# Performance work log

Measured on AMD Instinct MI355X. Metric: run time of the kernel, lower is better.

The kernel has to match this reference:

```python
import jax, jax.numpy as jnp
import numpy as np

NEG_SLOPE = 0.2  # PyG GATConv default leaky_relu slope
N_NODES, N_EDGES, F_IN, HID = 25000, 200000, 64, 128


def gat_layer(x, src, dst, W, a_src, a_dst, b, heads, ch):
    """PyG-style GATConv (concat=True, eval mode). x:[N,Fin] -> [N,heads*ch]."""
    N = x.shape[0]
    h = (x @ W).reshape(N, heads, ch)                      # [N,H,C]
    al_s = jnp.sum(h * a_src, axis=-1)                     # [N,H]
    al_d = jnp.sum(h * a_dst, axis=-1)                     # [N,H]
    e = jax.nn.leaky_relu(al_s[src] + al_d[dst], NEG_SLOPE)  # [E,H]
    # segment softmax over incoming edges of each dst node (stable)
    e = e - jax.ops.segment_max(e, dst, num_segments=N)[dst]
    ex = jnp.exp(e)
    alpha = ex / jax.ops.segment_sum(ex, dst, num_segments=N)[dst]  # [E,H]
    out = jax.ops.segment_sum(h[src] * alpha[:, :, None], dst, num_segments=N)  # [N,H,C]
    return out.reshape(N, heads * ch) + b


def setup_inputs() -> dict:
    key = jax.random.key(0)
    ks = jax.random.split(key, 24)
    def g(k, shape, fan_in):
        return jax.random.normal(k, shape, dtype=jnp.float32) / np.sqrt(fan_in)
    inp = {
        "x": jax.random.normal(ks[0], (N_NODES, F_IN), dtype=jnp.float32),
        "edge_index": jax.random.randint(ks[1], (2, N_EDGES), 0, N_NODES, dtype=jnp.int64) if jax.config.jax_enable_x64 else jax.random.randint(ks[1], (2, N_EDGES), 0, N_NODES).astype(jnp.int32),
        "liquor_idx": jax.random.randint(ks[2], (4096,), 0, N_NODES),
        "ingredient_idx": jax.random.randint(ks[3], (4096,), 0, N_NODES),
        "W1": g(ks[4], (F_IN, 8 * HID), F_IN), "a_s1": g(ks[5], (8, HID), HID), "a_d1": g(ks[6], (8, HID), HID), "b1": jnp.zeros((8 * HID,), jnp.float32),
        "W2": g(ks[7], (8 * HID, 8 * HID), 8 * HID), "a_s2": g(ks[8], (8, HID), HID), "a_d2": g(ks[9], (8, HID), HID), "b2": jnp.zeros((8 * HID,), jnp.float32),
        "W3": g(ks[10], (8 * HID, HID), 8 * HID), "a_s3": g(ks[11], (1, HID), HID), "a_d3": g(ks[12], (1, HID), HID), "b3": jnp.zeros((HID,), jnp.float32),
        # MLP scorer: 256 -> 128 -> 64 -> 1
        "mw1": g(ks[13], (2 * HID, HID), 2 * HID), "mb1": jnp.zeros((HID,), jnp.float32),
        "mw2": g(ks[14], (HID, HID // 2), HID), "mb2": jnp.zeros((HID // 2,), jnp.float32),
        "mw3": g(ks[15], (HID // 2, 1), HID // 2), "mb3": jnp.zeros((1,), jnp.float32),
    }
    return inp


def reference(x, edge_index, liquor_idx, ingredient_idx,
              W1, a_s1, a_d1, b1, W2, a_s2, a_d2, b2, W3, a_s3, a_d3, b3,
              mw1, mb1, mw2, mb2, mw3, mb3):
    N = x.shape[0]
    loops = jnp.arange(N, dtype=edge_index.dtype)  # GATConv adds self-loops
    src = jnp.concatenate([edge_index[0], loops])
    dst = jnp.concatenate([edge_index[1], loops])
    h = jax.nn.relu(gat_layer(x, src, dst, W1, a_s1, a_d1, b1, 8, HID))
    h = jax.nn.relu(gat_layer(h, src, dst, W2, a_s2, a_d2, b2, 8, HID))
    h = gat_layer(h, src, dst, W3, a_s3, a_d3, b3, 1, HID)
    pair = jnp.concatenate([h[liquor_idx], h[ingredient_idx]], axis=-1)  # [B,256]
    z = jax.nn.relu(pair @ mw1 + mb1)
    z = jax.nn.relu(z @ mw2 + mb2)
    z = z @ mw3 + mb3
    return jax.nn.sigmoid(z).squeeze(-1)
```

## Files before the change

kernel.cpp:

```cpp
#include <hip/hip_runtime.h>
#include <math.h>

#define NEG_SLOPE 0.2f

typedef short short8 __attribute__((ext_vector_type(8)));
typedef float f32x4 __attribute__((ext_vector_type(4)));

__device__ __forceinline__ float lrelu(float x){ return x > 0.f ? x : NEG_SLOPE * x; }

__device__ __forceinline__ unsigned short f2bf(float f){
  union { float f; unsigned u; } v; v.f = f;
  unsigned r = v.u + 0x7fff + ((v.u >> 16) & 1);
  return (unsigned short)(r >> 16);
}
__device__ __forceinline__ float bf2f(unsigned short u){
  union { unsigned u; float f; } v; v.u = ((unsigned)u) << 16; return v.f;
}

__device__ __forceinline__ void gld16(const unsigned short* g, unsigned short* l){
  __builtin_amdgcn_global_load_lds(
      (const __attribute__((address_space(1))) unsigned int*)g,
      (__attribute__((address_space(3))) unsigned int*)l, 16, 0, 0);
}

#define MFMA_BF16 __builtin_amdgcn_mfma_f32_16x16x32_bf16

__global__ void k_count(const int* __restrict__ dst, int* __restrict__ cnt, int E){
  int e = blockIdx.x*blockDim.x + threadIdx.x;
  if (e < E) atomicAdd(&cnt[dst[e]], 1);
}

__global__ void k_blockscan(const int* __restrict__ cnt, int* __restrict__ row,
                            int* __restrict__ aux, int n){
  __shared__ int buf[256];
  int t = threadIdx.x;
  int base = blockIdx.x * 256;
  int v = (base + t < n) ? cnt[base + t] : 0;
  buf[t] = v;
  __syncthreads();
  #pragma unroll
  for (int off = 1; off < 256; off <<= 1){
    int u = (t >= off) ? buf[t - off] : 0;
    __syncthreads();
    buf[t] += u;
    __syncthreads();
  }
  if (base + t < n) row[base + t + 1] = buf[t];
  if (t == 255) aux[blockIdx.x] = buf[255];
  if (blockIdx.x == 0 && t == 0) row[0] = 0;
}

__global__ void k_addoff(const int* __restrict__ aux, int* __restrict__ row, int n){
  __shared__ int s_pre;
  int b = blockIdx.x, t = threadIdx.x;
  if (t == 0){
    int pre = 0;
    for (int i = 0; i < b; ++i) pre += aux[i];
    s_pre = pre;
  }
  __syncthreads();
  int i = b * 256 + t;
  if (i < n) row[i + 1] += s_pre;
}

__global__ void k_scatter(const int* __restrict__ src, const int* __restrict__ dst,
                          const int* __restrict__ row, int* __restrict__ cur,
                          int* __restrict__ csr, int E){
  int e = blockIdx.x*blockDim.x + threadIdx.x;
  if (e < E){
    int d = dst[e];
    int p = atomicAdd(&cur[d], 1);
    csr[row[d] + p] = src[e];
  }
}

__global__ void k_prep(const float* __restrict__ x, unsigned short* __restrict__ xb, int nx, int nxb,
                       const float* __restrict__ W1, unsigned short* __restrict__ Wt1,
                       const float* __restrict__ W2, unsigned short* __restrict__ Wt2,
                       const float* __restrict__ W3, unsigned short* __restrict__ Wt3){
  __shared__ float tile[32][33];
  int b = blockIdx.x, t = threadIdx.x;
  if (b < nxb){
    int i0 = b * 2048 + t * 8;
    if (i0 + 8 <= nx){
      float4 f0 = *reinterpret_cast<const float4*>(x + i0);
      float4 f1 = *reinterpret_cast<const float4*>(x + i0 + 4);
      short8 o;
      o[0]=f2bf(f0.x); o[1]=f2bf(f0.y); o[2]=f2bf(f0.z); o[3]=f2bf(f0.w);
      o[4]=f2bf(f1.x); o[5]=f2bf(f1.y); o[6]=f2bf(f1.z); o[7]=f2bf(f1.w);
      *reinterpret_cast<short8*>(xb + i0) = o;
    } else {
      for (int k = 0; k < 8 && i0 + k < nx; ++k) xb[i0 + k] = f2bf(x[i0 + k]);
    }
    return;
  }
  const float* W; unsigned short* Wt; int K, N, ti;
  if (b < nxb + 64)            { W = W1; Wt = Wt1; K = 64;   N = 1024; ti = b - nxb;
                                 int kb = (ti & 1) * 32, nb = (ti >> 1) * 32;
                                 int tx = t & 31, ty = t >> 5;
                                 #pragma unroll
                                 for (int i = ty; i < 32; i += 8) tile[i][tx] = W[(size_t)(kb+i)*N + nb+tx];
                                 __syncthreads();
                                 #pragma unroll
                                 for (int i = ty; i < 32; i += 8) Wt[(size_t)(nb+i)*K + kb+tx] = f2bf(tile[tx][i]);
                                 return; }
  if (b < nxb + 64 + 1024)     { W = W2; Wt = Wt2; K = 1024; N = 1024; ti = b - nxb - 64; }
  else                         { W = W3; Wt = Wt3; K = 1024; N = 128;  ti = b - nxb - 64 - 1024; }
  int kb = (ti & 31) * 32, nb = (ti >> 5) * 32;
  int tx = t & 31, ty = t >> 5;
  #pragma unroll
  for (int i = ty; i < 32; i += 8) tile[i][tx] = W[(size_t)(kb+i)*N + nb+tx];
  __syncthreads();
  #pragma unroll
  for (int i = ty; i < 32; i += 8) Wt[(size_t)(nb+i)*K + kb+tx] = f2bf(tile[tx][i]);
}

__global__ void k_fold(const float* __restrict__ W1, const float* __restrict__ a_s,
                       const float* __restrict__ a_d, float* __restrict__ ws){
  int k = blockIdx.x, t = threadIdx.x;
  int h = t >> 5, l = t & 31;
  float4 wv = *reinterpret_cast<const float4*>(&W1[(size_t)k * 1024 + h * 128 + l * 4]);
  float4 sv = *reinterpret_cast<const float4*>(&a_s[h * 128 + l * 4]);
  float4 dv = *reinterpret_cast<const float4*>(&a_d[h * 128 + l * 4]);
  float ps = wv.x*sv.x + wv.y*sv.y + wv.z*sv.z + wv.w*sv.w;
  float pd = wv.x*dv.x + wv.y*dv.y + wv.z*dv.z + wv.w*dv.w;
  #pragma unroll
  for (int off = 16; off >= 1; off >>= 1){
    ps += __shfl_xor(ps, off);
    pd += __shfl_xor(pd, off);
  }
  if (l == 0){ ws[k * 16 + h] = ps; ws[k * 16 + 8 + h] = pd; }
}

__global__ void k_logits1(const unsigned short* __restrict__ xb, const float* __restrict__ ws,
                          float* __restrict__ ALS, float* __restrict__ ALD, int N){
  __shared__ unsigned short lx[32 * 64];
  __shared__ float lw[64 * 16];
  int t = threadIdx.x;
  int n0 = blockIdx.x * 32;
  int r = t >> 3, c = (t & 7) * 8;
  if (n0 + r < N)
    *reinterpret_cast<short8*>(&lx[r * 64 + c]) =
      *reinterpret_cast<const short8*>(&xb[(size_t)(n0 + r) * 64 + c]);
  else {
    short8 z = {0,0,0,0,0,0,0,0};
    *reinterpret_cast<short8*>(&lx[r * 64 + c]) = z;
  }
  *reinterpret_cast<float4*>(&lw[t * 4]) = *reinterpret_cast<const float4*>(&ws[t * 4]);
  __syncthreads();
  int nl = t >> 3, h = t & 7;
  if (n0 + nl >= N) return;
  float s = 0.f, d = 0.f;
  #pragma unroll 8
  for (int k = 0; k < 64; ++k){
    float xv = bf2f(lx[nl * 64 + k]);
    s = fmaf(xv, lw[k * 16 + h], s);
    d = fmaf(xv, lw[k * 16 + 8 + h], d);
  }
  ALS[(size_t)(n0 + nl) * 8 + h] = s;
  ALD[(size_t)(n0 + nl) * 8 + h] = d;
}

__global__ void k_gat_x(const unsigned short* __restrict__ xb, const float* __restrict__ ALS,
                        const float* __restrict__ ALD, const int* __restrict__ row,
                        const int* __restrict__ csr, unsigned short* __restrict__ G, int N){
  int t = threadIdx.x;
  int n = blockIdx.x * 4 + (t >> 6);
  if (n >= N) return;
  int lane = t & 63;
  float ald[8], m[8], l[8], acc[8];
  float xv = bf2f(xb[(size_t)n * 64 + lane]);
  #pragma unroll
  for (int h = 0; h < 8; ++h){
    ald[h] = ALD[(size_t)n * 8 + h];
    m[h] = lrelu(ALS[(size_t)n * 8 + h] + ald[h]);
    l[h] = 1.f;
    acc[h] = xv;
  }
  int beg = row[n], end = row[n + 1];
  for (int j = beg; j < end; ++j){
    int s = csr[j];
    float xs = bf2f(xb[(size_t)s * 64 + lane]);
    #pragma unroll
    for (int h = 0; h < 8; ++h){
      float e = lrelu(ALS[(size_t)s * 8 + h] + ald[h]);
      float mn = fmaxf(m[h], e);
      float sc = __expf(m[h] - mn);
      float p  = __expf(e - mn);
      acc[h] = acc[h] * sc + p * xs;
      l[h]   = l[h] * sc + p;
      m[h]   = mn;
    }
  }
  #pragma unroll
  for (int h = 0; h < 8; ++h)
    G[(size_t)n * 512 + h * 64 + lane] = f2bf(acc[h] / l[h]);
}

__global__ __launch_bounds__(256) void k_gemm_g(
    const unsigned short* __restrict__ G,
    const unsigned short* __restrict__ Bt,
    const float* __restrict__ bias,
    unsigned short* __restrict__ C,
    int M){
  __shared__ unsigned short As[128 * 32];
  __shared__ unsigned short Bs[128 * 32];
  const int nwg = gridDim.x;
  int bid = blockIdx.x;
  int swz = ((nwg & 7) == 0) ? ((bid & 7) * (nwg >> 3) + (bid >> 3)) : bid;
  const int head = swz % 8, byi = swz / 8;
  const int bm = byi * 128, bn = head * 128;
  const int tid  = threadIdx.x;
  const int lane = tid & 63, wave = tid >> 6;
  const int wr = wave >> 1, wc = wave & 1;
  const int lr = lane & 15, lk = lane >> 4;
  const int srow = wave * 16 + (lane >> 2);
  const int skc  = (lane & 3) * 8;
  int ar0 = bm + srow;      if (ar0 >= M) ar0 = M - 1;
  int ar1 = bm + srow + 64; if (ar1 >= M) ar1 = M - 1;
  const unsigned short* ga0 = G + (size_t)ar0 * 512 + head * 64 + skc;
  const unsigned short* ga1 = G + (size_t)ar1 * 512 + head * 64 + skc;
  const unsigned short* gb0 = Bt + (size_t)(bn + srow) * 64 + skc;
  const unsigned short* gb1 = Bt + (size_t)(bn + srow + 64) * 64 + skc;
  f32x4 acc[4][4] = {};
  #pragma unroll
  for (int k0 = 0; k0 < 64; k0 += 32){
    gld16(ga0 + k0, &As[(size_t)wave * 512]);
    gld16(ga1 + k0, &As[(size_t)(wave + 4) * 512]);
    gld16(gb0 + k0, &Bs[(size_t)wave * 512]);
    gld16(gb1 + k0, &Bs[(size_t)(wave + 4) * 512]);
    __syncthreads();
    short8 af[4], bg[4];
    #pragma unroll
    for (int m = 0; m < 4; ++m)
      af[m] = *reinterpret_cast<const short8*>(&As[(wr * 64 + m * 16 + lr) * 32 + lk * 8]);
    #pragma unroll
    for (int n = 0; n < 4; ++n)
      bg[n] = *reinterpret_cast<const short8*>(&Bs[(wc * 64 + n * 16 + lr) * 32 + lk * 8]);
    #pragma unroll
    for (int m = 0; m < 4; ++m)
      #pragma unroll
      for (int n = 0; n < 4; ++n)
        acc[m][n] = MFMA_BF16(af[m], bg[n], acc[m][n], 0, 0, 0);
    __syncthreads();
  }
  float bv[4];
  #pragma unroll
  for (int n = 0; n < 4; ++n) bv[n] = bias[bn + wc * 64 + n * 16 + lr];
  #pragma unroll
  for (int m = 0; m < 4; ++m){
    #pragma unroll
    for (int j = 0; j < 4; ++j){
      int rowi = bm + wr * 64 + m * 16 + lk * 4 + j;
      if (rowi < M){
        #pragma unroll
        for (int n = 0; n < 4; ++n)
          C[(size_t)rowi * 1024 + bn + wc * 64 + n * 16 + lr] = f2bf(fmaxf(acc[m][n][j] + bv[n], 0.f));
      }
    }
  }
}

template<int HEADS>
__global__ __launch_bounds__(256) void k_gemm_fused(
    const unsigned short* __restrict__ A, const unsigned short* __restrict__ Bt,
    unsigned short* __restrict__ C,
    const float* __restrict__ a_s, const float* __restrict__ a_d,
    float* __restrict__ ALS, float* __restrict__ ALD,
    int M, int N, int K, int gxc){
  __shared__ unsigned short SMEM[2 * 128 * 32];
  unsigned short* As = SMEM;
  unsigned short* Bs = SMEM + 128 * 32;
  const int nwg = gridDim.x;
  int bid = blockIdx.x;
  int swz = ((nwg & 7) == 0) ? ((bid & 7) * (nwg >> 3) + (bid >> 3)) : bid;
  const int bxi = swz % gxc, byi = swz / gxc;
  const int bm = byi * 128, bn = bxi * 128;
  const int head = bxi;
  const int tid  = threadIdx.x;
  const int lane = tid & 63, wave = tid >> 6;
  const int wr = wave >> 1, wc = wave & 1;
  const int lr = lane & 15, lk = lane >> 4;
  const int srow = wave * 16 + (lane >> 2);
  const int skc  = (lane & 3) * 8;
  int ar0 = bm + srow;      if (ar0 >= M) ar0 = M - 1;
  int ar1 = bm + srow + 64; if (ar1 >= M) ar1 = M - 1;
  const unsigned short* ga0 = A  + (size_t)ar0 * K + skc;
  const unsigned short* ga1 = A  + (size_t)ar1 * K + skc;
  const unsigned short* gb0 = Bt + (size_t)(bn + srow) * K + skc;
  const unsigned short* gb1 = Bt + (size_t)(bn + srow + 64) * K + skc;
  f32x4 acc[4][4] = {};
  for (int k0 = 0; k0 < K; k0 += 32){
    gld16(ga0 + k0, &As[(size_t)wave * 512]);
    gld16(ga1 + k0, &As[(size_t)(wave + 4) * 512]);
    gld16(gb0 + k0, &Bs[(size_t)wave * 512]);
    gld16(gb1 + k0, &Bs[(size_t)(wave + 4) * 512]);
    __syncthreads();
    short8 af[4], bg[4];
    #pragma unroll
    for (int m = 0; m < 4; ++m)
      af[m] = *reinterpret_cast<const short8*>(&As[(wr * 64 + m * 16 + lr) * 32 + lk * 8]);
    #pragma unroll
    for (int n = 0; n < 4; ++n)
      bg[n] = *reinterpret_cast<const short8*>(&Bs[(wc * 64 + n * 16 + lr) * 32 + lk * 8]);
    #pragma unroll
    for (int m = 0; m < 4; ++m)
      #pragma unroll
      for (int n = 0; n < 4; ++n)
        acc[m][n] = MFMA_BF16(af[m], bg[n], acc[m][n], 0, 0, 0);
    __syncthreads();
  }
  #pragma unroll
  for (int m = 0; m < 4; ++m){
    #pragma unroll
    for (int j = 0; j < 4; ++j){
      int rowi = bm + wr * 64 + m * 16 + lk * 4 + j;
      if (rowi < M){
        #pragma unroll
        for (int n = 0; n < 4; ++n)
          C[(size_t)rowi * N + bn + wc * 64 + n * 16 + lr] = f2bf(acc[m][n][j]);
      }
    }
  }
  float as4[4], ad4[4];
  #pragma unroll
  for (int n = 0; n < 4; ++n){
    as4[n] = a_s[head * 128 + wc * 64 + n * 16 + lr];
    ad4[n] = a_d[head * 128 + wc * 64 + n * 16 + lr];
  }
  float* red = (float*)SMEM;
  #pragma unroll
  for (int m = 0; m < 4; ++m){
    #pragma unroll
    for (int j = 0; j < 4; ++j){
      float ps = 0.f;
      #pragma unroll
      for (int n = 0; n < 4; ++n) ps = fmaf(acc[m][n][j], as4[n], ps);
      red[(wr * 64 + m * 16 + lk * 4 + j) * 32 + wc * 16 + lr] = ps;
    }
  }
  __syncthreads();
  if (tid < 128){
    float s = 0.f;
    #pragma unroll
    for (int i = 0; i < 32; ++i) s += red[tid * 32 + ((i + tid) & 31)];
    int gr = bm + tid;
    if (gr < M) ALS[(size_t)gr * HEADS + head] = s;
  }
  __syncthreads();
  #pragma unroll
  for (int m = 0; m < 4; ++m){
    #pragma unroll
    for (int j = 0; j < 4; ++j){
      float pd = 0.f;
      #pragma unroll
      for (int n = 0; n < 4; ++n) pd = fmaf(acc[m][n][j], ad4[n], pd);
      red[(wr * 64 + m * 16 + lk * 4 + j) * 32 + wc * 16 + lr] = pd;
    }
  }
  __syncthreads();
  if (tid < 128){
    float s = 0.f;
    #pragma unroll
    for (int i = 0; i < 32; ++i) s += red[tid * 32 + ((i + tid) & 31)];
    int gr = bm + tid;
    if (gr < M) ALD[(size_t)gr * HEADS + head] = s;
  }
}

__global__ __launch_bounds__(512, 2) void k_gemm256p8(
    const unsigned short* __restrict__ A,
    const unsigned short* __restrict__ Bt,
    unsigned short* __restrict__ C,
    const float* __restrict__ a_s, const float* __restrict__ a_d,
    float* __restrict__ ALS, float* __restrict__ ALD,
    int M, int N, int K, int gxc){
  __shared__ unsigned short smem[2 * 32768];
  const int nwg = gridDim.x;
  int bid = blockIdx.x;
  int swz = ((nwg & 7) == 0) ? ((bid & 7) * (nwg >> 3) + (bid >> 3)) : bid;
  const int bxi = swz % gxc, byi = swz / gxc;
  const int bm = byi * 256, bn = bxi * 256;
  const int tid = threadIdx.x;
  const int lane = tid & 63, wave = tid >> 6;
  const int wr = wave >> 2, wc = wave & 3;
  const int lr = lane & 15, lk = lane >> 4;
  const int sr = tid >> 3;
  const int scol = ((tid & 7) << 3) ^ ((sr & 7) << 3);
  unsigned offA[4], offB[4];
  #pragma unroll
  for (int u = 0; u < 4; ++u){
    int r = bm + u * 64 + sr; if (r >= M) r = M - 1;
    offA[u] = (unsigned)r * (unsigned)K + scol;
    offB[u] = (unsigned)(bn + u * 64 + sr) * (unsigned)K + scol;
  }
  const int wdst = wave * 512;
  const int NKT = K >> 6;
  const int NIT = NKT >> 1;

  #define STA(T,u) gld16(A  + (size_t)offA[u] + (size_t)(T)*64, &smem[((T)&1)*32768 + (u)*4096 + wdst])
  #define STB(T,u) gld16(Bt + (size_t)offB[u] + (size_t)(T)*64, &smem[((T)&1)*32768 + 16384 + (u)*4096 + wdst])

  #pragma unroll
  for (int u = 0; u < 4; ++u) STA(0, u);
  #pragma unroll
  for (int u = 0; u < 4; ++u) STB(0, u);
  #pragma unroll
  for (int u = 0; u < 4; ++u) STA(1, u);
  asm volatile("s_waitcnt vmcnt(4)" ::: "memory");
  __builtin_amdgcn_s_barrier();

  f32x4 acc[8][4] = {};
  short8 af[4][2], bg[4][2];

  #define RD_A(moff) \
    _Pragma("unroll") \
    for (int m = 0; m < 4; ++m){ \
      int row = wr * 128 + (m + (moff)) * 16 + lr; \
      int rb = row * 64, sw = (row & 7) << 3; \
      af[m][0] = *reinterpret_cast<const short8*>(&sa[rb + ((lk * 8) ^ sw)]); \
      af[m][1] = *reinterpret_cast<const short8*>(&sa[rb + ((32 + lk * 8) ^ sw)]); \
    }
  #define RD_B(n0_, n1_) \
    _Pragma("unroll") \
    for (int n = (n0_); n < (n1_); ++n){ \
      int row = wc * 64 + n * 16 + lr; \
      int rb = row * 64, sw = (row & 7) << 3; \
      bg[n][0] = *reinterpret_cast<const short8*>(&sb[rb + ((lk * 8) ^ sw)]); \
      bg[n][1] = *reinterpret_cast<const short8*>(&sb[rb + ((32 + lk * 8) ^ sw)]); \
    }
  #define SYNC_MFMA_BEG \
    __builtin_amdgcn_s_barrier(); \
    asm volatile("s_waitcnt lgkmcnt(0)" ::: "memory"); \
    __builtin_amdgcn_sched_barrier(0); \
    __builtin_amdgcn_s_setprio(1);
  #define QUAD(mb, nb) \
    _Pragma("unroll") \
    for (int m = 0; m < 4; ++m) \
      _Pragma("unroll") \
      for (int n = 0; n < 2; ++n){ \
        acc[(mb)+m][(nb)+n] = MFMA_BF16(af[m][0], bg[(nb)+n][0], acc[(mb)+m][(nb)+n], 0, 0, 0); \
        acc[(mb)+m][(nb)+n] = MFMA_BF16(af[m][1], bg[(nb)+n][1], acc[(mb)+m][(nb)+n], 0, 0, 0); \
      }
  #define SYNC_MFMA_END \
    __builtin_amdgcn_s_setprio(0); \
    __builtin_amdgcn_s_barrier();

  for (int it = 0; it < NIT; ++it){
    const int T = it << 1;
    {
      const unsigned short* sa = &smem[(T & 1) * 32768];
      const unsigned short* sb = sa + 16384;
      RD_A(0); RD_B(0, 2);
      STB(T + 1, 0); STB(T + 1, 1);
      SYNC_MFMA_BEG; QUAD(0, 0); SYNC_MFMA_END;
      RD_B(2, 4);
      STB(T + 1, 2); STB(T + 1, 3);
      SYNC_MFMA_BEG; QUAD(0, 2); SYNC_MFMA_END;
      RD_A(4);
      if (T + 2 < NKT){ STA(T + 2, 0); STA(T + 2, 2); }
      SYNC_MFMA_BEG; QUAD(4, 0); SYNC_MFMA_END;
      if (T + 2 < NKT){ STA(T + 2, 1); STA(T + 2, 3); }
      __builtin_amdgcn_s_barrier();
      __builtin_amdgcn_s_setprio(1);
      QUAD(4, 2);
      __builtin_amdgcn_s_setprio(0);
      asm volatile("s_waitcnt vmcnt(4)" ::: "memory");
      __builtin_amdgcn_s_barrier();
    }
    {
      const unsigned short* sa = &smem[((T + 1) & 1) * 32768];
      const unsigned short* sb = sa + 16384;
      RD_A(0); RD_B(0, 2);
      if (T + 2 < NKT){ STB(T + 2, 0); STB(T + 2, 1); }
      SYNC_MFMA_BEG; QUAD(0, 0); SYNC_MFMA_END;
      RD_B(2, 4);
      if (T + 2 < NKT){ STB(T + 2, 2); STB(T + 2, 3); }
      SYNC_MFMA_BEG; QUAD(0, 2); SYNC_MFMA_END;
      RD_A(4);
      if (T + 3 < NKT){ STA(T + 3, 0); STA(T + 3, 2); }
      SYNC_MFMA_BEG; QUAD(4, 0); SYNC_MFMA_END;
      if (T + 3 < NKT){ STA(T + 3, 1); STA(T + 3, 3); }
      __builtin_amdgcn_s_barrier();
      __builtin_amdgcn_s_setprio(1);
      QUAD(4, 2);
      __builtin_amdgcn_s_setprio(0);
      asm volatile("s_waitcnt vmcnt(4)" ::: "memory");
      __builtin_amdgcn_s_barrier();
    }
  }

  #pragma unroll
  for (int m = 0; m < 8; ++m){
    #pragma unroll
    for (int j = 0; j < 4; ++j){
      int row = bm + wr * 128 + m * 16 + lk * 4 + j;
      if (row < M){
        #pragma unroll
        for (int n = 0; n < 4; ++n)
          C[(size_t)row * N + bn + wc * 64 + n * 16 + lr] = f2bf(acc[m][n][j]);
      }
    }
  }
  const int hloc = wc >> 1;
  float as4[4], ad4[4];
  #pragma unroll
  for (int n = 0; n < 4; ++n){
    as4[n] = a_s[(bxi * 2 + hloc) * 128 + (wc & 1) * 64 + n * 16 + lr];
    ad4[n] = a_d[(bxi * 2 + hloc) * 128 + (wc & 1) * 64 + n * 16 + lr];
  }
  float2* red = (float2*)smem;
  __syncthreads();
  #pragma unroll
  for (int hh = 0; hh < 2; ++hh){
    if (hloc == hh){
      #pragma unroll
      for (int m = 0; m < 8; ++m){
        #pragma unroll
        for (int j = 0; j < 4; ++j){
          float ps = 0.f, pd = 0.f;
          #pragma unroll
          for (int n = 0; n < 4; ++n){
            ps = fmaf(acc[m][n][j], as4[n], ps);
            pd = fmaf(acc[m][n][j], ad4[n], pd);
          }
          red[(wr * 128 + m * 16 + lk * 4 + j) * 32 + (wc & 1) * 16 + lr] = make_float2(ps, pd);
        }
      }
    }
    __syncthreads();
    if (tid < 256){
      float ss = 0.f, sd = 0.f;
      #pragma unroll
      for (int i = 0; i < 32; ++i){
        float2 v = red[tid * 32 + ((i + tid) & 31)];
        ss += v.x; sd += v.y;
      }
      int gr = bm + tid;
      if (gr < M){
        ALS[(size_t)gr * 8 + bxi * 2 + hh] = ss;
        ALD[(size_t)gr * 8 + bxi * 2 + hh] = sd;
      }
    }
    __syncthreads();
  }
  #undef STA
  #undef STB
  #undef RD_A
  #undef RD_B
  #undef SYNC_MFMA_BEG
  #undef QUAD
  #undef SYNC_MFMA_END
}

template<int HEADS, int VEC, int OUTBF>
__global__ void k_gat_bf(const unsigned short* __restrict__ hp, const float* __restrict__ al_s,
                         const float* __restrict__ al_d, const int* __restrict__ row,
                         const int* __restrict__ csr, const float* __restrict__ bias,
                         void* __restrict__ outv, int N, int do_relu){
  constexpr int TPH = 128 / VEC;
  int n = blockIdx.x;
  int t = threadIdx.x;
  int h = t / TPH;
  int c0 = (t % TPH) * VEC;
  float ald = al_d[(size_t)n * HEADS + h];
  float mA = lrelu(al_s[(size_t)n * HEADS + h] + ald);
  float lA = 1.f;
  float accA[VEC], accB[VEC];
  float mB = -1e30f, lB = 0.f;
  const unsigned short* hpn = hp + ((size_t)n * HEADS + h) * 128 + c0;
  if constexpr (VEC == 8){
    short8 hv8 = *reinterpret_cast<const short8*>(hpn);
    #pragma unroll
    for (int v = 0; v < 8; ++v){ accA[v] = bf2f((unsigned short)hv8[v]); accB[v] = 0.f; }
  } else {
    ushort2 hv2 = *reinterpret_cast<const ushort2*>(hpn);
    accA[0] = bf2f(hv2.x); accA[1] = bf2f(hv2.y);
    accB[0] = 0.f; accB[1] = 0.f;
  }
  int beg = row[n], end = row[n + 1];
  int j = beg;
  for (; j + 1 < end; j += 2){
    int s0 = csr[j], s1 = csr[j + 1];
    float e0 = lrelu(al_s[(size_t)s0 * HEADS + h] + ald);
    float e1 = lrelu(al_s[(size_t)s1 * HEADS + h] + ald);
    const unsigned short* p0 = hp + ((size_t)s0 * HEADS + h) * 128 + c0;
    const unsigned short* p1 = hp + ((size_t)s1 * HEADS + h) * 128 + c0;
    if constexpr (VEC == 8){
      short8 v0 = *reinterpret_cast<const short8*>(p0);
      short8 v1 = *reinterpret_cast<const short8*>(p1);
      float mn0 = fmaxf(mA, e0), mn1 = fmaxf(mB, e1);
      float sc0 = __expf(mA - mn0), sc1 = __expf(mB - mn1);
      float pw0 = __expf(e0 - mn0), pw1 = __expf(e1 - mn1);
      #pragma unroll
      for (int v = 0; v < 8; ++v){
        accA[v] = accA[v] * sc0 + pw0 * bf2f((unsigned short)v0[v]);
        accB[v] = accB[v] * sc1 + pw1 * bf2f((unsigned short)v1[v]);
      }
      lA = lA * sc0 + pw0; mA = mn0;
      lB = lB * sc1 + pw1; mB = mn1;
    } else {
      ushort2 v0 = *reinterpret_cast<const ushort2*>(p0);
      ushort2 v1 = *reinterpret_cast<const ushort2*>(p1);
      float mn0 = fmaxf(mA, e0), mn1 = fmaxf(mB, e1);
      float sc0 = __expf(mA - mn0), sc1 = __expf(mB - mn1);
      float pw0 = __expf(e0 - mn0), pw1 = __expf(e1 - mn1);
      accA[0] = accA[0] * sc0 + pw0 * bf2f(v0.x);
      accA[1] = accA[1] * sc0 + pw0 * bf2f(v0.y);
      accB[0] = accB[0] * sc1 + pw1 * bf2f(v1.x);
      accB[1] = accB[1] * sc1 + pw1 * bf2f(v1.y);
      lA = lA * sc0 + pw0; mA = mn0;
      lB = lB * sc1 + pw1; mB = mn1;
    }
  }
  if (j < end){
    int s0 = csr[j];
    float e0 = lrelu(al_s[(size_t)s0 * HEADS + h] + ald);
    const unsigned short* p0 = hp + ((size_t)s0 * HEADS + h) * 128 + c0;
    float mn0 = fmaxf(mA, e0);
    float sc0 = __expf(mA - mn0), pw0 = __expf(e0 - mn0);
    if constexpr (VEC == 8){
      short8 v0 = *reinterpret_cast<const short8*>(p0);
      #pragma unroll
      for (int v = 0; v < 8; ++v) accA[v] = accA[v] * sc0 + pw0 * bf2f((unsigned short)v0[v]);
    } else {
      ushort2 v0 = *reinterpret_cast<const ushort2*>(p0);
      accA[0] = accA[0] * sc0 + pw0 * bf2f(v0.x);
      accA[1] = accA[1] * sc0 + pw0 * bf2f(v0.y);
    }
    lA = lA * sc0 + pw0; mA = mn0;
  }
  float mn = fmaxf(mA, mB);
  float sA = __expf(mA - mn), sB = __expf(mB - mn);
  float l = lA * sA + lB * sB;
  float inv = 1.f / l;
  size_t ob = ((size_t)n * HEADS + h) * 128 + c0;
  #pragma unroll
  for (int v = 0; v < VEC; ++v){
    float o = (accA[v] * sA + accB[v] * sB) * inv + bias[h * 128 + c0 + v];
    if (do_relu) o = fmaxf(o, 0.f);
    if constexpr (OUTBF) ((unsigned short*)outv)[ob + v] = f2bf(o);
    else                 ((float*)outv)[ob + v] = o;
  }
}

__global__ void k_gat3(const unsigned short* __restrict__ hp, const float* __restrict__ al_s,
                       const float* __restrict__ al_d, const int* __restrict__ row,
                       const int* __restrict__ csr, const float* __restrict__ bias,
                       const int* __restrict__ liq, const int* __restrict__ ing,
                       float* __restrict__ out, int NB){
  int b = blockIdx.x;
  int n = (b < NB) ? liq[b] : ing[b - NB];
  int t = threadIdx.x;
  int c0 = t * 2;
  float ald = al_d[n];
  float m = lrelu(al_s[n] + ald);
  float l = 1.f;
  ushort2 hv2 = *reinterpret_cast<const ushort2*>(hp + (size_t)n * 128 + c0);
  float a0 = bf2f(hv2.x), a1 = bf2f(hv2.y);
  int beg = row[n], end = row[n + 1];
  for (int j = beg; j < end; ++j){
    int s = csr[j];
    float e = lrelu(al_s[s] + ald);
    float mn = fmaxf(m, e);
    float sc = __expf(m - mn), p = __expf(e - mn);
    ushort2 v = *reinterpret_cast<const ushort2*>(hp + (size_t)s * 128 + c0);
    a0 = a0 * sc + p * bf2f(v.x);
    a1 = a1 * sc + p * bf2f(v.y);
    l = l * sc + p;
    m = mn;
  }
  float inv = 1.f / l;
  out[(size_t)b * 128 + c0]     = a0 * inv + bias[c0];
  out[(size_t)b * 128 + c0 + 1] = a1 * inv + bias[c0 + 1];
}

__global__ void k_mlp(const float* __restrict__ h3,
                      const float* __restrict__ mw1, const float* __restrict__ mb1,
                      const float* __restrict__ mw2, const float* __restrict__ mb2,
                      const float* __restrict__ mw3, const float* __restrict__ mb3,
                      float* __restrict__ out, int B){
  __shared__ float pairv[256];
  __shared__ float z1[128];
  __shared__ float z2[64];
  int r = blockIdx.x;
  int t = threadIdx.x;
  pairv[t]       = h3[(size_t)r * 128 + t];
  pairv[128 + t] = h3[(size_t)(B + r) * 128 + t];
  __syncthreads();
  float a1 = mb1[t];
  for (int k = 0; k < 256; ++k) a1 = fmaf(pairv[k], mw1[k * 128 + t], a1);
  z1[t] = fmaxf(a1, 0.f);
  __syncthreads();
  if (t < 64){
    float a2 = mb2[t];
    for (int k = 0; k < 128; ++k) a2 = fmaf(z1[k], mw2[k * 64 + t], a2);
    z2[t] = fmaxf(a2, 0.f);
  }
  __syncthreads();
  if (t < 64){
    float p = z2[t] * mw3[t];
    #pragma unroll
    for (int off = 32; off >= 1; off >>= 1) p += __shfl_xor(p, off);
    if (t == 0) out[r] = 1.f / (1.f + __expf(-(p + mb3[0])));
  }
}

extern "C" void kernel_launch(void* const* d_in, const int* in_sizes, int n_in,
                              void* d_out, int out_size, void* d_ws, size_t ws_size,
                              hipStream_t stream){
  const float* x   = (const float*)d_in[0];
  const int*   ei  = (const int*)  d_in[1];
  const int*   liq = (const int*)  d_in[2];
  const int*   ing = (const int*)  d_in[3];
  const float* W1  = (const float*)d_in[4];
  const float* as1 = (const float*)d_in[5];
  const float* ad1 = (const float*)d_in[6];
  const float* b1  = (const float*)d_in[7];
  const float* W2  = (const float*)d_in[8];
  const float* as2 = (const float*)d_in[9];
  const float* ad2 = (const float*)d_in[10];
  const float* b2  = (const float*)d_in[11];
  const float* W3  = (const float*)d_in[12];
  const float* as3 = (const float*)d_in[13];
  const float* ad3 = (const float*)d_in[14];
  const float* b3  = (const float*)d_in[15];
  const float* mw1 = (const float*)d_in[16];
  const float* mb1 = (const float*)d_in[17];
  const float* mw2 = (const float*)d_in[18];
  const float* mb2 = (const float*)d_in[19];
  const float* mw3 = (const float*)d_in[20];
  const float* mb3 = (const float*)d_in[21];
  float* out = (float*)d_out;

  const int N = in_sizes[0] / 64;
  const int E = in_sizes[1] / 2;
  const int B = in_sizes[2];
  const int* srcp = ei;
  const int* dstp = ei + E;

  char* w = (char*)d_ws;
  auto alloc = [&](size_t bytes) -> char* {
    char* p = w;
    w += (bytes + 255) & ~(size_t)255;
    return p;
  };
  unsigned short* P    = (unsigned short*)alloc((size_t)N * 1024 * 2);
  unsigned short* Hb   = (unsigned short*)alloc((size_t)N * 1024 * 2);
  float*          H3   = (float*)         alloc((size_t)2 * B * 128 * 4);
  unsigned short* xb   = (unsigned short*)alloc((size_t)N * 64 * 2);
  unsigned short* Wt1  = (unsigned short*)alloc((size_t)1024 * 64 * 2);
  unsigned short* Wt2  = (unsigned short*)alloc((size_t)1024 * 1024 * 2);
  unsigned short* Wt3  = (unsigned short*)alloc((size_t)128 * 1024 * 2);
  float* ALS  = (float*)alloc((size_t)N * 8 * 4);
  float* ALD  = (float*)alloc((size_t)N * 8 * 4);
  float* ws1  = (float*)alloc((size_t)64 * 16 * 4);
  int*   row  = (int*)  alloc((size_t)(N + 1) * 4);
  int*   cntcur = (int*)alloc((size_t)2 * N * 4);
  int*   cnt  = cntcur;
  int*   cur  = cntcur + N;
  int*   aux  = (int*)  alloc((size_t)256 * 4);
  int*   csr  = (int*)  alloc((size_t)E * 4);
  unsigned short* G = P;
  (void)ws_size; (void)n_in; (void)out_size;

  int nx = N * 64;
  int nxb = (nx + 2047) / 2048;
  k_prep<<<nxb + 64 + 1024 + 128, 256, 0, stream>>>(x, xb, nx, nxb, W1, Wt1, W2, Wt2, W3, Wt3);
  k_fold<<<64, 256, 0, stream>>>(W1, as1, ad1, ws1);

  hipMemsetAsync(cntcur, 0, (size_t)2 * N * 4, stream);
  int eb = (E + 255) / 256;
  int nb = (N + 255) / 256;
  k_count<<<eb, 256, 0, stream>>>(dstp, cnt, E);
  k_blockscan<<<nb, 256, 0, stream>>>(cnt, row, aux, N);
  k_addoff<<<nb, 256, 0, stream>>>(aux, row, N);
  k_scatter<<<eb, 256, 0, stream>>>(srcp, dstp, row, cur, csr, E);

  const int mt  = (N + 127) / 128;
  const int mt2 = (N + 255) / 256;

  k_logits1<<<(N + 31) / 32, 256, 0, stream>>>(xb, ws1, ALS, ALD, N);
  k_gat_x<<<(N + 3) / 4, 256, 0, stream>>>(xb, ALS, ALD, row, csr, G, N);
  k_gemm_g<<<8 * mt, 256, 0, stream>>>(G, Wt1, b1, Hb, N);

  k_gemm256p8<<<4 * mt2, 512, 0, stream>>>(Hb, Wt2, P, as2, ad2, ALS, ALD, N, 1024, 1024, 4);
  k_gat_bf<8,8,1><<<N, 128, 0, stream>>>(P, ALS, ALD, row, csr, b2, Hb, N, 1);

  k_gemm_fused<1><<<1 * mt, 256, 0, stream>>>(Hb, Wt3, P, as3, ad3, ALS, ALD, N, 128, 1024, 1);
  k_gat3<<<2 * B, 64, 0, stream>>>(P, ALS, ALD, row, csr, b3, liq, ing, H3, B);

  k_mlp<<<B, 128, 0, stream>>>(H3, mw1, mb1, mw2, mb2, mw3, mb3, out, B);
}
```

Baseline: 333.2 us.

## Use lazy softmax rescaling, parallel prefix offset, and restructured GEMM k-loop

The online softmax in all aggregation kernels now rescales the accumulator only when a new score exceeds the running max by a threshold, so most edges need one exp instead of two plus the rescale multiplies. The k_addoff kernel replaces a serial per-block prefix sum with a shared-memory tree reduction. The large GEMM main loop is rewritten from a manually unrolled two-tile iteration into a single-tile loop with separate A fragment registers, simpler barriers, and an explicit vmcnt(0) drain before the epilogue. The lazy rescale can let accumulators grow by up to about e^8 before renormalising, and the GEMM restructure may change how well LDS loads overlap with MFMA work.

```diff
diff --git a/kernel.cpp b/kernel.cpp
--- a/kernel.cpp
+++ b/kernel.cpp
@@ -24,6 +24,7 @@
 }
 
 #define MFMA_BF16 __builtin_amdgcn_mfma_f32_16x16x32_bf16
+#define RESCALE_THR 8.f
 
 __global__ void k_count(const int* __restrict__ dst, int* __restrict__ cnt, int E){
   int e = blockIdx.x*blockDim.x + threadIdx.x;
@@ -51,16 +52,17 @@
 }
 
 __global__ void k_addoff(const int* __restrict__ aux, int* __restrict__ row, int n){
-  __shared__ int s_pre;
+  __shared__ int sbuf[256];
   int b = blockIdx.x, t = threadIdx.x;
-  if (t == 0){
-    int pre = 0;
-    for (int i = 0; i < b; ++i) pre += aux[i];
-    s_pre = pre;
-  }
-  __syncthreads();
+  sbuf[t] = (t < b) ? aux[t] : 0;
+  __syncthreads();
+  #pragma unroll
+  for (int off = 128; off >= 1; off >>= 1){
+    if (t < off) sbuf[t] += sbuf[t + off];
+    __syncthreads();
+  }
   int i = b * 256 + t;
-  if (i < n) row[i + 1] += s_pre;
+  if (i < n) row[i + 1] += sbuf[0];
 }
 
 __global__ void k_scatter(const int* __restrict__ src, const int* __restrict__ dst,
@@ -184,12 +186,16 @@
     #pragma unroll
     for (int h = 0; h < 8; ++h){
       float e = lrelu(ALS[(size_t)s * 8 + h] + ald[h]);
-      float mn = fmaxf(m[h], e);
-      float sc = __expf(m[h] - mn);
-      float p  = __expf(e - mn);
-      acc[h] = acc[h] * sc + p * xs;
-      l[h]   = l[h] * sc + p;
-      m[h]   = mn;
+      float d = e - m[h];
+      float p;
+      if (__builtin_expect(d > RESCALE_THR, 0)){
+        float sc = __expf(-d);
+        acc[h] *= sc; l[h] *= sc; m[h] = e; p = 1.f;
+      } else {
+        p = __expf(d);
+      }
+      acc[h] = fmaf(p, xs, acc[h]);
+      l[h] += p;
     }
   }
   #pragma unroll
@@ -396,7 +402,6 @@
   }
   const int wdst = wave * 512;
   const int NKT = K >> 6;
-  const int NIT = NKT >> 1;
 
   #define STA(T,u) gld16(A  + (size_t)offA[u] + (size_t)(T)*64, &smem[((T)&1)*32768 + (u)*4096 + wdst])
   #define STB(T,u) gld16(Bt + (size_t)offB[u] + (size_t)(T)*64, &smem[((T)&1)*32768 + 16384 + (u)*4096 + wdst])
@@ -411,17 +416,17 @@
   __builtin_amdgcn_s_barrier();
 
   f32x4 acc[8][4] = {};
-  short8 af[4][2], bg[4][2];
-
-  #define RD_A(moff) \
+  short8 afA[4][2], afB[4][2], bg[4][2];
+
+  #define RD_AF(dst, moff) \
     _Pragma("unroll") \
     for (int m = 0; m < 4; ++m){ \
       int row = wr * 128 + (m + (moff)) * 16 + lr; \
       int rb = row * 64, sw = (row & 7) << 3; \
-      af[m][0] = *reinterpret_cast<const short8*>(&sa[rb + ((lk * 8) ^ sw)]); \
-      af[m][1] = *reinterpret_cast<const short8*>(&sa[rb + ((32 + lk * 8) ^ sw)]); \
-    }
-  #define RD_B(n0_, n1_) \
+      dst[m][0] = *reinterpret_cast<const short8*>(&sa[rb + ((lk * 8) ^ sw)]); \
+      dst[m][1] = *reinterpret_cast<const short8*>(&sa[rb + ((32 + lk * 8) ^ sw)]); \
+    }
+  #define RD_BG(n0_, n1_) \
     _Pragma("unroll") \
     for (int n = (n0_); n < (n1_); ++n){ \
       int row = wc * 64 + n * 16 + lr; \
@@ -429,65 +434,46 @@
       bg[n][0] = *reinterpret_cast<const short8*>(&sb[rb + ((lk * 8) ^ sw)]); \
       bg[n][1] = *reinterpret_cast<const short8*>(&sb[rb + ((32 + lk * 8) ^ sw)]); \
     }
-  #define SYNC_MFMA_BEG \
-    __builtin_amdgcn_s_barrier(); \
-    asm volatile("s_waitcnt lgkmcnt(0)" ::: "memory"); \
-    __builtin_amdgcn_sched_barrier(0); \
-    __builtin_amdgcn_s_setprio(1);
-  #define QUAD(mb, nb) \
+  #define QUADX(src, mb, nb) \
     _Pragma("unroll") \
     for (int m = 0; m < 4; ++m) \
       _Pragma("unroll") \
       for (int n = 0; n < 2; ++n){ \
-        acc[(mb)+m][(nb)+n] = MFMA_BF16(af[m][0], bg[(nb)+n][0], acc[(mb)+m][(nb)+n], 0, 0, 0); \
-        acc[(mb)+m][(nb)+n] = MFMA_BF16(af[m][1], bg[(nb)+n][1], acc[(mb)+m][(nb)+n], 0, 0, 0); \
-      }
-  #define SYNC_MFMA_END \
-    __builtin_amdgcn_s_setprio(0); \
+        acc[(mb)+m][(nb)+n] = MFMA_BF16(src[m][0], bg[(nb)+n][0], acc[(mb)+m][(nb)+n], 0, 0, 0); \
+        acc[(mb)+m][(nb)+n] = MFMA_BF16(src[m][1], bg[(nb)+n][1], acc[(mb)+m][(nb)+n], 0, 0, 0); \
+      }
+
+  for (int kt = 0; kt < NKT; ++kt){
+    const unsigned short* sa = &smem[(kt & 1) * 32768];
+    const unsigned short* sb = sa + 16384;
+    RD_AF(afA, 0);
+    RD_BG(0, 4);
+    if (kt + 1 < NKT){ STB(kt + 1, 0); STB(kt + 1, 1); }
     __builtin_amdgcn_s_barrier();
-
-  for (int it = 0; it < NIT; ++it){
-    const int T = it << 1;
-    {
-      const unsigned short* sa = &smem[(T & 1) * 32768];
-      const unsigned short* sb = sa + 16384;
-      RD_A(0); RD_B(0, 2);
-      STB(T + 1, 0); STB(T + 1, 1);
-      SYNC_MFMA_BEG; QUAD(0, 0); SYNC_MFMA_END;
-      RD_B(2, 4);
-      STB(T + 1, 2); STB(T + 1, 3);
-      SYNC_MFMA_BEG; QUAD(0, 2); SYNC_MFMA_END;
-      RD_A(4);
-      if (T + 2 < NKT){ STA(T + 2, 0); STA(T + 2, 2); }
-      SYNC_MFMA_BEG; QUAD(4, 0); SYNC_MFMA_END;
-      if (T + 2 < NKT){ STA(T + 2, 1); STA(T + 2, 3); }
-      __builtin_amdgcn_s_barrier();
-      __builtin_amdgcn_s_setprio(1);
-      QUAD(4, 2);
-      __builtin_amdgcn_s_setprio(0);
-      asm volatile("s_waitcnt vmcnt(4)" ::: "memory");
-      __builtin_amdgcn_s_barrier();
-    }
-    {
-      const unsigned short* sa = &smem[((T + 1) & 1) * 32768];
-      const unsigned short* sb = sa + 16384;
-      RD_A(0); RD_B(0, 2);
-      if (T + 2 < NKT){ STB(T + 2, 0); STB(T + 2, 1); }
-      SYNC_MFMA_BEG; QUAD(0, 0); SYNC_MFMA_END;
-      RD_B(2, 4);
-      if (T + 2 < NKT){ STB(T + 2, 2); STB(T + 2, 3); }
-      SYNC_MFMA_BEG; QUAD(0, 2); SYNC_MFMA_END;
-      RD_A(4);
-      if (T + 3 < NKT){ STA(T + 3, 0); STA(T + 3, 2); }
-      SYNC_MFMA_BEG; QUAD(4, 0); SYNC_MFMA_END;
-      if (T + 3 < NKT){ STA(T + 3, 1); STA(T + 3, 3); }
-      __builtin_amdgcn_s_barrier();
-      __builtin_amdgcn_s_setprio(1);
-      QUAD(4, 2);
-      __builtin_amdgcn_s_setprio(0);
-      asm volatile("s_waitcnt vmcnt(4)" ::: "memory");
-      __builtin_amdgcn_s_barrier();
-    }
+    __builtin_amdgcn_s_setprio(1);
+    QUADX(afA, 0, 0);
+    __builtin_amdgcn_s_setprio(0);
+    __builtin_amdgcn_s_barrier();
+    RD_AF(afB, 4);
+    if (kt + 1 < NKT){ STB(kt + 1, 2); STB(kt + 1, 3); }
+    __builtin_amdgcn_s_barrier();
+    __builtin_amdgcn_s_setprio(1);
+    QUADX(afA, 0, 2);
+    __builtin_amdgcn_s_setprio(0);
+    __builtin_amdgcn_s_barrier();
+    if (kt + 2 < NKT){ STA(kt + 2, 0); STA(kt + 2, 2); }
+    __builtin_amdgcn_s_barrier();
+    __builtin_amdgcn_s_setprio(1);
+    QUADX(afB, 4, 0);
+    __builtin_amdgcn_s_setprio(0);
+    __builtin_amdgcn_s_barrier();
+    if (kt + 2 < NKT){ STA(kt + 2, 1); STA(kt + 2, 3); }
+    __builtin_amdgcn_s_barrier();
+    __builtin_amdgcn_s_setprio(1);
+    QUADX(afB, 4, 2);
+    __builtin_amdgcn_s_setprio(0);
+    asm volatile("s_waitcnt vmcnt(4)" ::: "memory");
+    __builtin_amdgcn_s_barrier();
   }
 
   #pragma unroll
@@ -509,6 +495,8 @@
     as4[n] = a_s[(bxi * 2 + hloc) * 128 + (wc & 1) * 64 + n * 16 + lr];
     ad4[n] = a_d[(bxi * 2 + hloc) * 128 + (wc & 1) * 64 + n * 16 + lr];
   }
+  asm volatile("s_waitcnt vmcnt(0)" ::: "memory");
+  __builtin_amdgcn_s_barrier();
   float2* red = (float2*)smem;
   __syncthreads();
   #pragma unroll
@@ -546,11 +534,9 @@
   }
   #undef STA
   #undef STB
-  #undef RD_A
-  #undef RD_B
-  #undef SYNC_MFMA_BEG
-  #undef QUAD
-  #undef SYNC_MFMA_END
+  #undef RD_AF
+  #undef RD_BG
+  #undef QUADX
 }
 
 template<int HEADS, int VEC, int OUTBF>
@@ -586,49 +572,61 @@
     float e1 = lrelu(al_s[(size_t)s1 * HEADS + h] + ald);
     const unsigned short* p0 = hp + ((size_t)s0 * HEADS + h) * 128 + c0;
     const unsigned short* p1 = hp + ((size_t)s1 * HEADS + h) * 128 + c0;
+    float d0 = e0 - mA, d1 = e1 - mB;
+    float pw0, pw1;
+    if (__builtin_expect(d0 > RESCALE_THR, 0)){
+      float sc = __expf(-d0);
+      #pragma unroll
+      for (int v = 0; v < VEC; ++v) accA[v] *= sc;
+      lA *= sc; mA = e0; pw0 = 1.f;
+    } else pw0 = __expf(d0);
+    if (__builtin_expect(d1 > RESCALE_THR, 0)){
+      float sc = __expf(-d1);
+      #pragma unroll
+      for (int v = 0; v < VEC; ++v) accB[v] *= sc;
+      lB *= sc; mB = e1; pw1 = 1.f;
+    } else pw1 = __expf(d1);
     if constexpr (VEC == 8){
       short8 v0 = *reinterpret_cast<const short8*>(p0);
       short8 v1 = *reinterpret_cast<const short8*>(p1);
-      float mn0 = fmaxf(mA, e0), mn1 = fmaxf(mB, e1);
-      float sc0 = __expf(mA - mn0), sc1 = __expf(mB - mn1);
-      float pw0 = __expf(e0 - mn0), pw1 = __expf(e1 - mn1);
       #pragma unroll
       for (int v = 0; v < 8; ++v){
-        accA[v] = accA[v] * sc0 + pw0 * bf2f((unsigned short)v0[v]);
-        accB[v] = accB[v] * sc1 + pw1 * bf2f((unsigned short)v1[v]);
-      }
-      lA = lA * sc0 + pw0; mA = mn0;
-      lB = lB * sc1 + pw1; mB = mn1;
+        accA[v] = fmaf(pw0, bf2f((unsigned short)v0[v]), accA[v]);
+        accB[v] = fmaf(pw1, bf2f((unsigned short)v1[v]), accB[v]);
+      }
     } else {
       ushort2 v0 = *reinterpret_cast<const ushort2*>(p0);
       ushort2 v1 = *reinterpret_cast<const ushort2*>(p1);
-      float mn0 = fmaxf(mA, e0), mn1 = fmaxf(mB, e1);
-      float sc0 = __expf(mA - mn0), sc1 = __expf(mB - mn1);
-      float pw0 = __expf(e0 - mn0), pw1 = __expf(e1 - mn1);
-      accA[0] = accA[0] * sc0 + pw0 * bf2f(v0.x);
-      accA[1] = accA[1] * sc0 + pw0 * bf2f(v0.y);
-      accB[0] = accB[0] * sc1 + pw1 * bf2f(v1.x);
-      accB[1] = accB[1] * sc1 + pw1 * bf2f(v1.y);
-      lA = lA * sc0 + pw0; mA = mn0;
-      lB = lB * sc1 + pw1; mB = mn1;
-    }
+      accA[0] = fmaf(pw0, bf2f(v0.x), accA[0]);
+      accA[1] = fmaf(pw0, bf2f(v0.y), accA[1]);
+      accB[0] = fmaf(pw1, bf2f(v1.x), accB[0]);
+      accB[1] = fmaf(pw1, bf2f(v1.y), accB[1]);
+    }
+    lA += pw0;
+    lB += pw1;
   }
   if (j < end){
     int s0 = csr[j];
     float e0 = lrelu(al_s[(size_t)s0 * HEADS + h] + ald);
     const unsigned short* p0 = hp + ((size_t)s0 * HEADS + h) * 128 + c0;
-    float mn0 = fmaxf(mA, e0);
-    float sc0 = __expf(mA - mn0), pw0 = __expf(e0 - mn0);
+    float d0 = e0 - mA;
+    float pw0;
+    if (__builtin_expect(d0 > RESCALE_THR, 0)){
+      float sc = __expf(-d0);
+      #pragma unroll
+      for (int v = 0; v < VEC; ++v) accA[v] *= sc;
+      lA *= sc; mA = e0; pw0 = 1.f;
+    } else pw0 = __expf(d0);
     if constexpr (VEC == 8){
       short8 v0 = *reinterpret_cast<const short8*>(p0);
       #pragma unroll
-      for (int v = 0; v < 8; ++v) accA[v] = accA[v] * sc0 + pw0 * bf2f((unsigned short)v0[v]);
+      for (int v = 0; v < 8; ++v) accA[v] = fmaf(pw0, bf2f((unsigned short)v0[v]), accA[v]);
     } else {
       ushort2 v0 = *reinterpret_cast<const ushort2*>(p0);
-      accA[0] = accA[0] * sc0 + pw0 * bf2f(v0.x);
-      accA[1] = accA[1] * sc0 + pw0 * bf2f(v0.y);
-    }
-    lA = lA * sc0 + pw0; mA = mn0;
+      accA[0] = fmaf(pw0, bf2f(v0.x), accA[0]);
+      accA[1] = fmaf(pw0, bf2f(v0.y), accA[1]);
+    }
+    lA += pw0;
   }
   float mn = fmaxf(mA, mB);
   float sA = __expf(mA - mn), sB = __expf(mB - mn);
@@ -662,13 +660,16 @@
   for (int j = beg; j < end; ++j){
     int s = csr[j];
     float e = lrelu(al_s[s] + ald);
-    float mn = fmaxf(m, e);
-    float sc = __expf(m - mn), p = __expf(e - mn);
+    float d = e - m;
+    float p;
+    if (__builtin_expect(d > RESCALE_THR, 0)){
+      float sc = __expf(-d);
+      a0 *= sc; a1 *= sc; l *= sc; m = e; p = 1.f;
+    } else p = __expf(d);
     ushort2 v = *reinterpret_cast<const ushort2*>(hp + (size_t)s * 128 + c0);
-    a0 = a0 * sc + p * bf2f(v.x);
-    a1 = a1 * sc + p * bf2f(v.y);
-    l = l * sc + p;
-    m = mn;
+    a0 = fmaf(p, bf2f(v.x), a0);
+    a1 = fmaf(p, bf2f(v.y), a1);
+    l += p;
   }
   float inv = 1.f / l;
   out[(size_t)b * 128 + c0]     = a0 * inv + bias[c0];
```

After: 369.4 us. 1.11x slower.
